# Kernel optimization log

Hardware: AMD Instinct MI355X
Metric: run time of the kernel (lower is better)

## Reference

```python
import jax, jax.numpy as jnp
import numpy as np

FD, FO, FK, H = 1024, 512, 128, 4
N = 32768


def setup_inputs() -> dict:
    key = jax.random.key(0)
    ks = jax.random.split(key, 8)
    s = 0.02
    return {
        "Xd": jax.random.normal(ks[0], (N, FD), dtype=jnp.float32),
        "Xo": jax.random.normal(ks[1], (N, FO), dtype=jnp.float32),
        "Wq": jax.random.normal(ks[2], (FO, FK * H), dtype=jnp.float32) * s,
        "bq": jnp.zeros((FK * H,), dtype=jnp.float32),
        "Wk": jax.random.normal(ks[3], (FD, FK * H), dtype=jnp.float32) * s,
        "bk": jnp.zeros((FK * H,), dtype=jnp.float32),
        "Wv": jax.random.normal(ks[4], (FD, FD * H), dtype=jnp.float32) * s,
        "bv": jnp.zeros((FD * H,), dtype=jnp.float32),
    }


def reference(Xd, Xo, Wq, bq, Wk, bk, Wv, bv):
    n = Xd.shape[0]
    Q = (Xo @ Wq + bq).reshape(n, H, FK)      # (n, H, fk)
    K = (Xd @ Wk + bk).reshape(n, H, FK)      # (n, H, fk)
    V = (Xd @ Wv + bv).reshape(n, H, FD)      # (n, H, fd)
    scores = jnp.sum(Q * K, axis=2, keepdims=True)  # (n, H, 1), no softmax
    Z = scores * V                              # (n, H, fd)
    Z = jnp.max(Z, axis=1)                      # max pooling over heads -> (n, fd)
    return Z  # dropout is identity in inference
```

## Files before the change

kernel.cpp:

```cpp
#include <hip/hip_runtime.h>

typedef __attribute__((ext_vector_type(8))) short short8;
typedef __attribute__((ext_vector_type(4))) float f32x4;

#define GLL16(gp, lp) __builtin_amdgcn_global_load_lds( \
    (__attribute__((address_space(1))) void*)(gp), \
    (__attribute__((address_space(3))) void*)(lp), 16, 0, 0)

__device__ __forceinline__ unsigned short f2b(float f) {
  unsigned int u = __builtin_bit_cast(unsigned int, f);
  u += 0x7fffu + ((u >> 16) & 1u);
  return (unsigned short)(u >> 16);
}
__device__ __forceinline__ float b2f(unsigned short s) {
  unsigned int u = ((unsigned int)s) << 16;
  return __builtin_bit_cast(float, u);
}

__global__ __launch_bounds__(256) void conv_k(const float* __restrict__ in,
                                              short8* __restrict__ out, long n8) {
  for (long i = (long)blockIdx.x * 256 + threadIdx.x; i < n8;
       i += (long)gridDim.x * 256) {
    const float4* p = (const float4*)in + 2 * i;
    float4 a = p[0], b = p[1];
    short8 v;
    v[0] = (short)f2b(a.x); v[1] = (short)f2b(a.y);
    v[2] = (short)f2b(a.z); v[3] = (short)f2b(a.w);
    v[4] = (short)f2b(b.x); v[5] = (short)f2b(b.y);
    v[6] = (short)f2b(b.z); v[7] = (short)f2b(b.w);
    out[i] = v;
  }
}

__global__ __launch_bounds__(256) void tconv_k(const float* __restrict__ in,
                                               unsigned short* __restrict__ out,
                                               int K, int C, int inter) {
  __shared__ float t[32][33];
  int k0 = blockIdx.x * 32, c0 = blockIdx.y * 32;
  int tx = threadIdx.x & 31, ty = threadIdx.x >> 5;
#pragma unroll
  for (int p = 0; p < 4; ++p)
    t[ty + p * 8][tx] = in[(size_t)(k0 + ty + p * 8) * C + c0 + tx];
  __syncthreads();
#pragma unroll
  for (int p = 0; p < 4; ++p) {
    int c = ty + p * 8;
    int gc = c0 + c;
    int orow = inter ? ((gc & 1023) * 4 + (gc >> 10)) : gc;
    out[(size_t)orow * K + k0 + tx] = f2b(t[tx][c]);
  }
}

template <int KD, int EPI>
__global__ __launch_bounds__(256) void gemm_k(
    const unsigned short* __restrict__ A, const unsigned short* __restrict__ Bt,
    const float* __restrict__ bias, const unsigned short* __restrict__ Qb,
    unsigned short* __restrict__ outb, float* __restrict__ sc,
    float* __restrict__ Z) {
  __shared__ __align__(16) unsigned short As[128 * 64];
  __shared__ __align__(16) unsigned short Bs[128 * 64];
  __shared__ float s_sc[512];
  __shared__ float sred[128][2];

  int tid = threadIdx.x;
  int bid = blockIdx.x;
  int ntile, mtile;
  if constexpr (EPI == 2) {
    int cpx = gridDim.x >> 3;
    int lb = (bid & 7) * cpx + (bid >> 3);
    ntile = lb & 31;
    mtile = lb >> 5;
  } else {
    ntile = bid & 3;
    mtile = bid >> 2;
  }
  int l = tid & 63, wid = tid >> 6, wm = wid >> 1, wn = wid & 1;
  int m0 = mtile * 128;

  if constexpr (EPI == 2) {
    for (int i = tid; i < 512; i += 256) s_sc[i] = sc[(size_t)m0 * 4 + i];
  }

  const unsigned short* Ab = A + (size_t)m0 * KD;
  const unsigned short* Bb = Bt + (size_t)ntile * 128 * KD;

  f32x4 zero = {0.f, 0.f, 0.f, 0.f};
  f32x4 acc[4][4];
#pragma unroll
  for (int m = 0; m < 4; ++m)
#pragma unroll
    for (int n = 0; n < 4; ++n) acc[m][n] = zero;

  for (int kt = 0; kt < KD / 64; ++kt) {
    const unsigned short* sA = Ab + kt * 64;
    const unsigned short* sB = Bb + kt * 64;
#pragma unroll
    for (int p = 0; p < 4; ++p) {
      int row = p * 32 + wid * 8 + (l >> 3);
      int sch = (l & 7) ^ (row & 7);
      GLL16((const char*)(sA + (size_t)row * KD) + sch * 16,
            (char*)As + p * 4096 + wid * 1024);
    }
#pragma unroll
    for (int p = 0; p < 4; ++p) {
      int row = p * 32 + wid * 8 + (l >> 3);
      int sch = (l & 7) ^ (row & 7);
      GLL16((const char*)(sB + (size_t)row * KD) + sch * 16,
            (char*)Bs + p * 4096 + wid * 1024);
    }
    __syncthreads();
#pragma unroll
    for (int ks = 0; ks < 2; ++ks) {
      short8 af[4], bfr[4];
#pragma unroll
      for (int m = 0; m < 4; ++m) {
        int row = wm * 64 + m * 16 + (l & 15);
        int kc = ks * 4 + (l >> 4);
        af[m] = *(const short8*)((const char*)As + row * 128 +
                                 ((kc ^ (row & 7)) << 4));
      }
#pragma unroll
      for (int n = 0; n < 4; ++n) {
        int row = wn * 64 + n * 16 + (l & 15);
        int kc = ks * 4 + (l >> 4);
        bfr[n] = *(const short8*)((const char*)Bs + row * 128 +
                                  ((kc ^ (row & 7)) << 4));
      }
#pragma unroll
      for (int m = 0; m < 4; ++m)
#pragma unroll
        for (int n = 0; n < 4; ++n)
          acc[m][n] = __builtin_amdgcn_mfma_f32_16x16x32_bf16(af[m], bfr[n],
                                                              acc[m][n], 0, 0, 0);
    }
    __syncthreads();
  }

  if constexpr (EPI == 0) {
#pragma unroll
    for (int n = 0; n < 4; ++n) {
      int col = ntile * 128 + wn * 64 + n * 16 + (l & 15);
      float bb = bias[col];
#pragma unroll
      for (int m = 0; m < 4; ++m) {
        int rowb = m0 + wm * 64 + m * 16 + ((l >> 4) << 2);
#pragma unroll
        for (int r = 0; r < 4; ++r)
          outb[(size_t)(rowb + r) * 512 + col] = f2b(acc[m][n][r] + bb);
      }
    }
  } else if constexpr (EPI == 1) {
    float part[4][4] = {};
#pragma unroll
    for (int n = 0; n < 4; ++n) {
      int col = ntile * 128 + wn * 64 + n * 16 + (l & 15);
      float bb = bias[col];
#pragma unroll
      for (int m = 0; m < 4; ++m) {
        int rowb = m0 + wm * 64 + m * 16 + ((l >> 4) << 2);
#pragma unroll
        for (int r = 0; r < 4; ++r) {
          float kv = acc[m][n][r] + bb;
          part[m][r] += kv * b2f(Qb[(size_t)(rowb + r) * 512 + col]);
        }
      }
    }
#pragma unroll
    for (int m = 0; m < 4; ++m)
#pragma unroll
      for (int r = 0; r < 4; ++r) {
        float s = part[m][r];
        s += __shfl_xor(s, 1);
        s += __shfl_xor(s, 2);
        s += __shfl_xor(s, 4);
        s += __shfl_xor(s, 8);
        if ((l & 15) == 0)
          sred[wm * 64 + m * 16 + ((l >> 4) << 2) + r][wn] = s;
      }
    __syncthreads();
    if (tid < 128) sc[(size_t)(m0 + tid) * 4 + ntile] = sred[tid][0] + sred[tid][1];
  } else {
    float* Zs = (float*)As;
#pragma unroll
    for (int n = 0; n < 4; ++n) {
      int pl = wn * 64 + n * 16 + (l & 15);
      int pg = ntile * 128 + pl;
      int h = pl & 3;
      float bb = bias[(pg & 3) * 1024 + (pg >> 2)];
#pragma unroll
      for (int m = 0; m < 4; ++m) {
        int rl = wm * 64 + m * 16 + ((l >> 4) << 2);
#pragma unroll
        for (int r = 0; r < 4; ++r) {
          float z = s_sc[(rl + r) * 4 + h] * (acc[m][n][r] + bb);
          z = fmaxf(z, __shfl_xor(z, 1));
          z = fmaxf(z, __shfl_xor(z, 2));
          if ((l & 3) == 0) Zs[(rl + r) * 32 + (pl >> 2)] = z;
        }
      }
    }
    __syncthreads();
#pragma unroll
    for (int p = 0; p < 4; ++p) {
      int idx = p * 1024 + tid * 4;
      int row = idx >> 5, d = idx & 31;
      f32x4 v = *(const f32x4*)&Zs[idx];
      *(f32x4*)&Z[(size_t)(m0 + row) * 1024 + ntile * 32 + d] = v;
    }
  }
}

__global__ __launch_bounds__(256) void naive_k(
    const float* __restrict__ Xd, const float* __restrict__ Xo,
    const float* __restrict__ Wq, const float* __restrict__ bq,
    const float* __restrict__ Wk, const float* __restrict__ bk,
    const float* __restrict__ Wv, const float* __restrict__ bv,
    float* __restrict__ Z) {
  int i = blockIdx.x, t = threadIdx.x;
  __shared__ float xd[1024], xo[512], s[4];
  for (int j = t; j < 1024; j += 256) xd[j] = Xd[(size_t)i * 1024 + j];
  for (int j = t; j < 512; j += 256) xo[j] = Xo[(size_t)i * 512 + j];
  if (t < 4) s[t] = 0.f;
  __syncthreads();
  for (int c = t; c < 512; c += 256) {
    float q = bq[c], k = bk[c];
    for (int j = 0; j < 512; ++j) q += xo[j] * Wq[(size_t)j * 512 + c];
    for (int j = 0; j < 1024; ++j) k += xd[j] * Wk[(size_t)j * 512 + c];
    atomicAdd(&s[c >> 7], q * k);
  }
  __syncthreads();
  for (int d = t; d < 1024; d += 256) {
    float z = -INFINITY;
    for (int h = 0; h < 4; ++h) {
      float v = bv[h * 1024 + d];
      for (int j = 0; j < 1024; ++j) v += xd[j] * Wv[(size_t)j * 4096 + h * 1024 + d];
      z = fmaxf(z, s[h] * v);
    }
    Z[(size_t)i * 1024 + d] = z;
  }
}

extern "C" void kernel_launch(void* const* d_in, const int* in_sizes, int n_in,
                              void* d_out, int out_size, void* d_ws, size_t ws_size,
                              hipStream_t stream) {
  const float* Xd = (const float*)d_in[0];
  const float* Xo = (const float*)d_in[1];
  const float* Wq = (const float*)d_in[2];
  const float* bq = (const float*)d_in[3];
  const float* Wk = (const float*)d_in[4];
  const float* bk = (const float*)d_in[5];
  const float* Wv = (const float*)d_in[6];
  const float* bv = (const float*)d_in[7];
  float* Z = (float*)d_out;
  long N = in_sizes[0] / 1024;

  size_t sz_Xd = (size_t)N * 1024 * 2, sz_Xo = (size_t)N * 512 * 2;
  size_t sz_Wq = (size_t)512 * 512 * 2, sz_Wk = (size_t)512 * 1024 * 2;
  size_t sz_Wv = (size_t)4096 * 1024 * 2;
  size_t sz_Qb = (size_t)N * 512 * 2, sz_sc = (size_t)N * 4 * 4;
  size_t o_Xo = sz_Xd, o_Wq = o_Xo + sz_Xo, o_Wk = o_Wq + sz_Wq,
         o_Wv = o_Wk + sz_Wk, o_Qb = o_Wv + sz_Wv, o_sc = o_Qb + sz_Qb;
  size_t need = o_sc + sz_sc;

  if (ws_size < need || (N % 128) != 0) {
    naive_k<<<(int)N, 256, 0, stream>>>(Xd, Xo, Wq, bq, Wk, bk, Wv, bv, Z);
    return;
  }

  char* w = (char*)d_ws;
  unsigned short* Xd_b = (unsigned short*)w;
  unsigned short* Xo_b = (unsigned short*)(w + o_Xo);
  unsigned short* Wq_t = (unsigned short*)(w + o_Wq);
  unsigned short* Wk_t = (unsigned short*)(w + o_Wk);
  unsigned short* Wv_p = (unsigned short*)(w + o_Wv);
  unsigned short* Qb   = (unsigned short*)(w + o_Qb);
  float* sc = (float*)(w + o_sc);

  conv_k<<<2048, 256, 0, stream>>>(Xd, (short8*)Xd_b, N * 1024 / 8);
  conv_k<<<2048, 256, 0, stream>>>(Xo, (short8*)Xo_b, N * 512 / 8);
  tconv_k<<<dim3(16, 16), 256, 0, stream>>>(Wq, Wq_t, 512, 512, 0);
  tconv_k<<<dim3(32, 16), 256, 0, stream>>>(Wk, Wk_t, 1024, 512, 0);
  tconv_k<<<dim3(32, 128), 256, 0, stream>>>(Wv, Wv_p, 1024, 4096, 1);

  int mt = (int)(N / 128);
  gemm_k<512, 0><<<mt * 4, 256, 0, stream>>>(Xo_b, Wq_t, bq, nullptr, Qb, nullptr, nullptr);
  gemm_k<1024, 1><<<mt * 4, 256, 0, stream>>>(Xd_b, Wk_t, bk, Qb, nullptr, sc, nullptr);
  gemm_k<1024, 2><<<mt * 32, 256, 0, stream>>>(Xd_b, Wv_p, bv, nullptr, nullptr, sc, Z);
}
```

Before: 565.7 us.

## Replace V GEMM with 256x256-tile double-buffered kernel using direct-to-LDS loads

The large V projection GEMM (N x 4096 x 1024) moves from a 128x128-tile, 256-thread kernel to a new 256x256-tile, 512-thread kernel. The new kernel double-buffers LDS tiles filled by global_load_lds, so the next K-step's loads overlap the current MFMAs, and raises MFMA wave priority with s_setprio. The larger tiles raise arithmetic intensity and cut redundant global reads of A and B. In exchange it uses more LDS (128KB of tiles) and more accumulator registers, limiting occupancy, and it now requires N to be a multiple of 256.

Measured after the change: 533.9 us. 5.6% less time.

```diff
diff --git a/kernel.cpp b/kernel.cpp
--- a/kernel.cpp
+++ b/kernel.cpp
@@ -51,35 +51,143 @@
   }
 }
 
+template <int KD>
+__global__ __launch_bounds__(512, 2) void gemm_v256_k(
+    const unsigned short* __restrict__ A, const unsigned short* __restrict__ Bt,
+    const float* __restrict__ bias, const float* __restrict__ sc,
+    float* __restrict__ Z) {
+  __shared__ __align__(16) unsigned short Ash[2][16384];
+  __shared__ __align__(16) unsigned short Bsh[2][16384];
+  __shared__ float s_sc[1024];
+
+  int tid = threadIdx.x;
+  int bid = blockIdx.x;
+  int cpx = gridDim.x >> 3;
+  int lb = (bid & 7) * cpx + (bid >> 3);
+  int mtile = lb >> 4, nt0 = lb & 15;
+  long m0 = (long)mtile * 256;
+  int l = tid & 63, wid = tid >> 6, wm = wid >> 2, wn = wid & 3;
+
+  for (int i = tid; i < 1024; i += 512) s_sc[i] = sc[m0 * 4 + i];
+
+  int rowg = tid >> 3;
+  int srcOff = rowg * (KD * 2) + (((tid & 7) ^ (rowg & 7)) << 4);
+  const char* aB = (const char*)(A + m0 * KD) + srcOff;
+  const char* bB = (const char*)(Bt + (long)nt0 * 256 * KD) + srcOff;
+  char* AshB = (char*)Ash;
+  char* BshB = (char*)Bsh;
+  int dstOff = wid * 1024;
+
+  auto stage = [&](int k, int bb) {
+#pragma unroll
+    for (int h = 0; h < 2; ++h)
+#pragma unroll
+      for (int s = 0; s < 2; ++s) {
+        int go = (h * 128 + s * 64) * (KD * 2) + k * 128;
+        int lo = bb * 32768 + h * 16384 + s * 8192 + dstOff;
+        GLL16(aB + go, AshB + lo);
+        GLL16(bB + go, BshB + lo);
+      }
+  };
+
+  f32x4 zero = {0.f, 0.f, 0.f, 0.f};
+  f32x4 acc[8][4];
+#pragma unroll
+  for (int m = 0; m < 8; ++m)
+#pragma unroll
+    for (int n = 0; n < 4; ++n) acc[m][n] = zero;
+
+  stage(0, 0);
+
+  const int NKT = KD / 64;
+  for (int kt = 0; kt < NKT; ++kt) {
+    int b = kt & 1;
+    asm volatile("s_waitcnt vmcnt(0)" ::: "memory");
+    __builtin_amdgcn_s_barrier();
+    __builtin_amdgcn_sched_barrier(0);
+    if (kt + 1 < NKT) stage(kt + 1, b ^ 1);
+
+    const char* Al = AshB + b * 32768;
+    const char* Bl = BshB + b * 32768;
+    int ar = l & 15;
+    int kc = l >> 4;
+    short8 bf[2][4], af[4];
+#pragma unroll
+    for (int ks = 0; ks < 2; ++ks) {
+#pragma unroll
+      for (int mh = 0; mh < 2; ++mh) {
+        if (mh == 0) {
+#pragma unroll
+          for (int n = 0; n < 4; ++n) {
+            int row = wn * 64 + n * 16 + ar;
+            int c = (ks * 4 + kc) ^ (row & 7);
+            bf[ks][n] = *(const short8*)(Bl + row * 128 + (c << 4));
+          }
+        }
+#pragma unroll
+        for (int m = 0; m < 4; ++m) {
+          int row = wm * 128 + mh * 64 + m * 16 + ar;
+          int c = (ks * 4 + kc) ^ (row & 7);
+          af[m] = *(const short8*)(Al + row * 128 + (c << 4));
+        }
+        __builtin_amdgcn_s_barrier();
+        __builtin_amdgcn_s_setprio(1);
+#pragma unroll
+        for (int m = 0; m < 4; ++m)
+#pragma unroll
+          for (int n = 0; n < 4; ++n)
+            acc[mh * 4 + m][n] = __builtin_amdgcn_mfma_f32_16x16x32_bf16(
+                af[m], bf[ks][n], acc[mh * 4 + m][n], 0, 0, 0);
+        __builtin_amdgcn_s_setprio(0);
+        __builtin_amdgcn_s_barrier();
+      }
+    }
+  }
+
+  __syncthreads();
+  float* Zs = (float*)AshB;
+#pragma unroll
+  for (int n = 0; n < 4; ++n) {
+    int pl = wn * 64 + n * 16 + (l & 15);
+    int pg = nt0 * 256 + pl;
+    int h = pl & 3;
+    float bb = bias[(pg & 3) * 1024 + (pg >> 2)];
+#pragma unroll
+    for (int mi = 0; mi < 8; ++mi) {
+      int rl = wm * 128 + mi * 16 + ((l >> 4) << 2);
+#pragma unroll
+      for (int r = 0; r < 4; ++r) {
+        float z = s_sc[(rl + r) * 4 + h] * (acc[mi][n][r] + bb);
+        z = fmaxf(z, __shfl_xor(z, 1));
+        z = fmaxf(z, __shfl_xor(z, 2));
+        if ((l & 3) == 0) Zs[(rl + r) * 64 + (pl >> 2)] = z;
+      }
+    }
+  }
+  __syncthreads();
+#pragma unroll
+  for (int it = 0; it < 8; ++it) {
+    int i = it * 512 + tid;
+    int row = i >> 4, d4 = i & 15;
+    f32x4 v = *(const f32x4*)&Zs[row * 64 + d4 * 4];
+    *(f32x4*)&Z[(m0 + row) * 1024 + nt0 * 64 + d4 * 4] = v;
+  }
+}
+
 template <int KD, int EPI>
 __global__ __launch_bounds__(256) void gemm_k(
     const unsigned short* __restrict__ A, const unsigned short* __restrict__ Bt,
     const float* __restrict__ bias, const unsigned short* __restrict__ Qb,
-    unsigned short* __restrict__ outb, float* __restrict__ sc,
-    float* __restrict__ Z) {
+    unsigned short* __restrict__ outb, float* __restrict__ sc) {
   __shared__ __align__(16) unsigned short As[128 * 64];
   __shared__ __align__(16) unsigned short Bs[128 * 64];
-  __shared__ float s_sc[512];
   __shared__ float sred[128][2];
 
   int tid = threadIdx.x;
   int bid = blockIdx.x;
-  int ntile, mtile;
-  if constexpr (EPI == 2) {
-    int cpx = gridDim.x >> 3;
-    int lb = (bid & 7) * cpx + (bid >> 3);
-    ntile = lb & 31;
-    mtile = lb >> 5;
-  } else {
-    ntile = bid & 3;
-    mtile = bid >> 2;
-  }
+  int ntile = bid & 3, mtile = bid >> 2;
   int l = tid & 63, wid = tid >> 6, wm = wid >> 1, wn = wid & 1;
   int m0 = mtile * 128;
-
-  if constexpr (EPI == 2) {
-    for (int i = tid; i < 512; i += 256) s_sc[i] = sc[(size_t)m0 * 4 + i];
-  }
 
   const unsigned short* Ab = A + (size_t)m0 * KD;
   const unsigned short* Bb = Bt + (size_t)ntile * 128 * KD;
@@ -149,7 +257,7 @@
           outb[(size_t)(rowb + r) * 512 + col] = f2b(acc[m][n][r] + bb);
       }
     }
-  } else if constexpr (EPI == 1) {
+  } else {
     float part[4][4] = {};
 #pragma unroll
     for (int n = 0; n < 4; ++n) {
@@ -179,34 +287,6 @@
       }
     __syncthreads();
     if (tid < 128) sc[(size_t)(m0 + tid) * 4 + ntile] = sred[tid][0] + sred[tid][1];
-  } else {
-    float* Zs = (float*)As;
-#pragma unroll
-    for (int n = 0; n < 4; ++n) {
-      int pl = wn * 64 + n * 16 + (l & 15);
-      int pg = ntile * 128 + pl;
-      int h = pl & 3;
-      float bb = bias[(pg & 3) * 1024 + (pg >> 2)];
-#pragma unroll
-      for (int m = 0; m < 4; ++m) {
-        int rl = wm * 64 + m * 16 + ((l >> 4) << 2);
-#pragma unroll
-        for (int r = 0; r < 4; ++r) {
-          float z = s_sc[(rl + r) * 4 + h] * (acc[m][n][r] + bb);
-          z = fmaxf(z, __shfl_xor(z, 1));
-          z = fmaxf(z, __shfl_xor(z, 2));
-          if ((l & 3) == 0) Zs[(rl + r) * 32 + (pl >> 2)] = z;
-        }
-      }
-    }
-    __syncthreads();
-#pragma unroll
-    for (int p = 0; p < 4; ++p) {
-      int idx = p * 1024 + tid * 4;
-      int row = idx >> 5, d = idx & 31;
-      f32x4 v = *(const f32x4*)&Zs[idx];
-      *(f32x4*)&Z[(size_t)(m0 + row) * 1024 + ntile * 32 + d] = v;
-    }
   }
 }
 
@@ -262,7 +342,7 @@
          o_Wv = o_Wk + sz_Wk, o_Qb = o_Wv + sz_Wv, o_sc = o_Qb + sz_Qb;
   size_t need = o_sc + sz_sc;
 
-  if (ws_size < need || (N % 128) != 0) {
+  if (ws_size < need || (N % 256) != 0) {
     naive_k<<<(int)N, 256, 0, stream>>>(Xd, Xo, Wq, bq, Wk, bk, Wv, bv, Z);
     return;
   }
@@ -283,7 +363,7 @@
   tconv_k<<<dim3(32, 128), 256, 0, stream>>>(Wv, Wv_p, 1024, 4096, 1);
 
   int mt = (int)(N / 128);
-  gemm_k<512, 0><<<mt * 4, 256, 0, stream>>>(Xo_b, Wq_t, bq, nullptr, Qb, nullptr, nullptr);
-  gemm_k<1024, 1><<<mt * 4, 256, 0, stream>>>(Xd_b, Wk_t, bk, Qb, nullptr, sc, nullptr);
-  gemm_k<1024, 2><<<mt * 32, 256, 0, stream>>>(Xd_b, Wv_p, bv, nullptr, nullptr, sc, Z);
-}
+  gemm_k<512, 0><<<mt * 4, 256, 0, stream>>>(Xo_b, Wq_t, bq, nullptr, Qb, nullptr);
+  gemm_k<1024, 1><<<mt * 4, 256, 0, stream>>>(Xd_b, Wk_t, bk, Qb, nullptr, sc);
+  gemm_v256_k<1024><<<(int)(N / 256) * 16, 512, 0, stream>>>(Xd_b, Wv_p, bv, sc, Z);
+}
```

## Pre-pack operands into MFMA fragment layout and load directly to registers

Applied to the files above, without the earlier changes.

Conversion kernels now write A and B in a fragment-major bf16 layout, so each lane's 16-byte MFMA operand sits contiguously in global memory. The GEMM drops shared-memory staging and barriers in the main loop, loading fragments straight into registers with software double-buffering. Tiles grow to 256x128 with 512 threads. Every operand is now fetched from global or L2 by each wave with no LDS reuse, which raises cache traffic and register pressure.

Result: slower. 707.8 us (+25.1%).

```diff
diff --git a/kernel.cpp b/kernel.cpp
--- a/kernel.cpp
+++ b/kernel.cpp
@@ -2,10 +2,6 @@
 
 typedef __attribute__((ext_vector_type(8))) short short8;
 typedef __attribute__((ext_vector_type(4))) float f32x4;
-
-#define GLL16(gp, lp) __builtin_amdgcn_global_load_lds( \
-    (__attribute__((address_space(1))) void*)(gp), \
-    (__attribute__((address_space(3))) void*)(lp), 16, 0, 0)
 
 __device__ __forceinline__ unsigned short f2b(float f) {
   unsigned int u = __builtin_bit_cast(unsigned int, f);
@@ -17,72 +13,96 @@
   return __builtin_bit_cast(float, u);
 }
 
-__global__ __launch_bounds__(256) void conv_k(const float* __restrict__ in,
-                                              short8* __restrict__ out, long n8) {
-  for (long i = (long)blockIdx.x * 256 + threadIdx.x; i < n8;
-       i += (long)gridDim.x * 256) {
-    const float4* p = (const float4*)in + 2 * i;
+__global__ __launch_bounds__(256) void pack_a_k(const float* __restrict__ in,
+                                                unsigned short* __restrict__ out, int K) {
+  int R = blockIdx.x, t = threadIdx.x;
+  int NS = K / 32;
+  for (int i = 0; i < K / 128; ++i) {
+    int c = t + 256 * i;
+    int S = c >> 6, l = c & 63;
+    int row = R * 16 + (l & 15);
+    int k = S * 32 + (l >> 4) * 8;
+    const float4* p = (const float4*)(in + (size_t)row * K + k);
     float4 a = p[0], b = p[1];
     short8 v;
     v[0] = (short)f2b(a.x); v[1] = (short)f2b(a.y);
     v[2] = (short)f2b(a.z); v[3] = (short)f2b(a.w);
     v[4] = (short)f2b(b.x); v[5] = (short)f2b(b.y);
     v[6] = (short)f2b(b.z); v[7] = (short)f2b(b.w);
-    out[i] = v;
-  }
-}
-
-__global__ __launch_bounds__(256) void tconv_k(const float* __restrict__ in,
-                                               unsigned short* __restrict__ out,
-                                               int K, int C, int inter) {
-  __shared__ float t[32][33];
-  int k0 = blockIdx.x * 32, c0 = blockIdx.y * 32;
-  int tx = threadIdx.x & 31, ty = threadIdx.x >> 5;
-#pragma unroll
-  for (int p = 0; p < 4; ++p)
-    t[ty + p * 8][tx] = in[(size_t)(k0 + ty + p * 8) * C + c0 + tx];
+    ((short8*)out)[(size_t)(R * NS + S) * 64 + l] = v;
+  }
+}
+
+template <int INTER>
+__global__ __launch_bounds__(256) void pack_b_k(const float* __restrict__ in,
+                                                unsigned short* __restrict__ out,
+                                                int K, int C) {
+  __shared__ float tl[128][17];
+  int P = blockIdx.x, kc = blockIdx.y, t = threadIdx.x;
+  int k0 = kc * 128;
+#pragma unroll
+  for (int ii = 0; ii < 2; ++ii) {
+    int id = t + 256 * ii;
+    int k = id >> 2, g = id & 3;
+    int cbase;
+    if (INTER) cbase = g * 1024 + P * 4;
+    else       cbase = P * 16 + g * 4;
+    float4 f = *(const float4*)(in + (size_t)(k0 + k) * C + cbase);
+#pragma unroll
+    for (int q = 0; q < 4; ++q) {
+      int pi = INTER ? (q * 4 + g) : (g * 4 + q);
+      tl[k][pi] = ((const float*)&f)[q];
+    }
+  }
   __syncthreads();
-#pragma unroll
-  for (int p = 0; p < 4; ++p) {
-    int c = ty + p * 8;
-    int gc = c0 + c;
-    int orow = inter ? ((gc & 1023) * 4 + (gc >> 10)) : gc;
-    out[(size_t)orow * K + k0 + tx] = f2b(t[tx][c]);
-  }
-}
-
-template <int KD, int EPI>
-__global__ __launch_bounds__(256) void gemm_k(
-    const unsigned short* __restrict__ A, const unsigned short* __restrict__ Bt,
+  int Sl = t >> 6, l = t & 63;
+  short8 v;
+#pragma unroll
+  for (int j = 0; j < 8; ++j)
+    v[j] = (short)f2b(tl[Sl * 32 + (l >> 4) * 8 + j][l & 15]);
+  int NS = K / 32;
+  ((short8*)out)[(size_t)(P * NS + kc * 4 + Sl) * 64 + l] = v;
+}
+
+template <int KD, int NTI, int EPI>
+__global__ __launch_bounds__(512, 3) void gemm_flat(
+    const unsigned short* __restrict__ Af, const unsigned short* __restrict__ Bf,
     const float* __restrict__ bias, const unsigned short* __restrict__ Qb,
     unsigned short* __restrict__ outb, float* __restrict__ sc,
     float* __restrict__ Z) {
-  __shared__ __align__(16) unsigned short As[128 * 64];
-  __shared__ __align__(16) unsigned short Bs[128 * 64];
-  __shared__ float s_sc[512];
-  __shared__ float sred[128][2];
+  constexpr int NS = KD / 32;
+  constexpr int SMB = (EPI == 2) ? (36864) : 2048;
+  __shared__ __align__(16) char smem[SMB];
 
   int tid = threadIdx.x;
   int bid = blockIdx.x;
-  int ntile, mtile;
+  int cpx = gridDim.x >> 3;
+  int lb = (bid & 7) * cpx + (bid >> 3);
+  int mtile = lb / NTI, nt = lb % NTI;
+  long m0 = (long)mtile * 256;
+  int l = tid & 63, wid = tid >> 6, wm = wid >> 1, wn = wid & 1;
+
+  float* s_sc = (float*)smem;
+  float* Zs = (float*)(smem + 4096);
+  float (*sred)[2] = (float(*)[2])smem;
+
   if constexpr (EPI == 2) {
-    int cpx = gridDim.x >> 3;
-    int lb = (bid & 7) * cpx + (bid >> 3);
-    ntile = lb & 31;
-    mtile = lb >> 5;
-  } else {
-    ntile = bid & 3;
-    mtile = bid >> 2;
-  }
-  int l = tid & 63, wid = tid >> 6, wm = wid >> 1, wn = wid & 1;
-  int m0 = mtile * 128;
-
-  if constexpr (EPI == 2) {
-    for (int i = tid; i < 512; i += 256) s_sc[i] = sc[(size_t)m0 * 4 + i];
-  }
-
-  const unsigned short* Ab = A + (size_t)m0 * KD;
-  const unsigned short* Bb = Bt + (size_t)ntile * 128 * KD;
+    for (int i = tid; i < 1024; i += 512) s_sc[i] = sc[m0 * 4 + i];
+  }
+
+  const char* Ab[4];
+  const char* Bb[4];
+#pragma unroll
+  for (int m = 0; m < 4; ++m) {
+    int R = (int)(m0 >> 4) + wm * 4 + m;
+    Ab[m] = (const char*)Af + (size_t)R * NS * 1024;
+  }
+#pragma unroll
+  for (int n = 0; n < 4; ++n) {
+    int P = nt * 8 + wn * 4 + n;
+    Bb[n] = (const char*)Bf + (size_t)P * NS * 1024;
+  }
+  int voff = l * 16;
 
   f32x4 zero = {0.f, 0.f, 0.f, 0.f};
   f32x4 acc[4][4];
@@ -91,77 +111,65 @@
 #pragma unroll
     for (int n = 0; n < 4; ++n) acc[m][n] = zero;
 
-  for (int kt = 0; kt < KD / 64; ++kt) {
-    const unsigned short* sA = Ab + kt * 64;
-    const unsigned short* sB = Bb + kt * 64;
-#pragma unroll
-    for (int p = 0; p < 4; ++p) {
-      int row = p * 32 + wid * 8 + (l >> 3);
-      int sch = (l & 7) ^ (row & 7);
-      GLL16((const char*)(sA + (size_t)row * KD) + sch * 16,
-            (char*)As + p * 4096 + wid * 1024);
-    }
-#pragma unroll
-    for (int p = 0; p < 4; ++p) {
-      int row = p * 32 + wid * 8 + (l >> 3);
-      int sch = (l & 7) ^ (row & 7);
-      GLL16((const char*)(sB + (size_t)row * KD) + sch * 16,
-            (char*)Bs + p * 4096 + wid * 1024);
-    }
-    __syncthreads();
-#pragma unroll
-    for (int ks = 0; ks < 2; ++ks) {
-      short8 af[4], bfr[4];
+#define LD4(dst, bases, add)                                              \
+  do {                                                                    \
+    _Pragma("unroll") for (int i_ = 0; i_ < 4; ++i_)                      \
+        dst[i_] = *(const short8*)(bases[i_] + voff + (add));             \
+  } while (0)
+#define MF(A_, B_)                                                        \
+  do {                                                                    \
+    _Pragma("unroll") for (int m_ = 0; m_ < 4; ++m_)                      \
+        _Pragma("unroll") for (int n_ = 0; n_ < 4; ++n_) acc[m_][n_] =    \
+            __builtin_amdgcn_mfma_f32_16x16x32_bf16(A_[m_], B_[n_],       \
+                                                    acc[m_][n_], 0, 0, 0);\
+  } while (0)
+
+  short8 a0[4], b0[4], a1[4], b1[4];
+  LD4(a0, Ab, 0);
+  LD4(b0, Bb, 0);
+  int off = 0;
+  for (int s = 0; s + 2 < NS; s += 2) {
+    LD4(a1, Ab, off + 1024);
+    LD4(b1, Bb, off + 1024);
+    MF(a0, b0);
+    LD4(a0, Ab, off + 2048);
+    LD4(b0, Bb, off + 2048);
+    MF(a1, b1);
+    off += 2048;
+  }
+  LD4(a1, Ab, off + 1024);
+  LD4(b1, Bb, off + 1024);
+  MF(a0, b0);
+  MF(a1, b1);
+#undef LD4
+#undef MF
+
+  if constexpr (EPI == 0) {
+#pragma unroll
+    for (int n = 0; n < 4; ++n) {
+      int col = nt * 128 + wn * 64 + n * 16 + (l & 15);
+      float bb = bias[col];
 #pragma unroll
       for (int m = 0; m < 4; ++m) {
-        int row = wm * 64 + m * 16 + (l & 15);
-        int kc = ks * 4 + (l >> 4);
-        af[m] = *(const short8*)((const char*)As + row * 128 +
-                                 ((kc ^ (row & 7)) << 4));
-      }
-#pragma unroll
-      for (int n = 0; n < 4; ++n) {
-        int row = wn * 64 + n * 16 + (l & 15);
-        int kc = ks * 4 + (l >> 4);
-        bfr[n] = *(const short8*)((const char*)Bs + row * 128 +
-                                  ((kc ^ (row & 7)) << 4));
-      }
-#pragma unroll
-      for (int m = 0; m < 4; ++m)
-#pragma unroll
-        for (int n = 0; n < 4; ++n)
-          acc[m][n] = __builtin_amdgcn_mfma_f32_16x16x32_bf16(af[m], bfr[n],
-                                                              acc[m][n], 0, 0, 0);
-    }
-    __syncthreads();
-  }
-
-  if constexpr (EPI == 0) {
-#pragma unroll
-    for (int n = 0; n < 4; ++n) {
-      int col = ntile * 128 + wn * 64 + n * 16 + (l & 15);
-      float bb = bias[col];
-#pragma unroll
-      for (int m = 0; m < 4; ++m) {
-        int rowb = m0 + wm * 64 + m * 16 + ((l >> 4) << 2);
+        long rowb = m0 + wm * 64 + m * 16 + ((l >> 4) << 2);
 #pragma unroll
         for (int r = 0; r < 4; ++r)
-          outb[(size_t)(rowb + r) * 512 + col] = f2b(acc[m][n][r] + bb);
+          outb[(rowb + r) * 512 + col] = f2b(acc[m][n][r] + bb);
       }
     }
   } else if constexpr (EPI == 1) {
     float part[4][4] = {};
 #pragma unroll
     for (int n = 0; n < 4; ++n) {
-      int col = ntile * 128 + wn * 64 + n * 16 + (l & 15);
+      int col = nt * 128 + wn * 64 + n * 16 + (l & 15);
       float bb = bias[col];
 #pragma unroll
       for (int m = 0; m < 4; ++m) {
-        int rowb = m0 + wm * 64 + m * 16 + ((l >> 4) << 2);
+        long rowb = m0 + wm * 64 + m * 16 + ((l >> 4) << 2);
 #pragma unroll
         for (int r = 0; r < 4; ++r) {
           float kv = acc[m][n][r] + bb;
-          part[m][r] += kv * b2f(Qb[(size_t)(rowb + r) * 512 + col]);
+          part[m][r] += kv * b2f(Qb[(rowb + r) * 512 + col]);
         }
       }
     }
@@ -178,14 +186,14 @@
           sred[wm * 64 + m * 16 + ((l >> 4) << 2) + r][wn] = s;
       }
     __syncthreads();
-    if (tid < 128) sc[(size_t)(m0 + tid) * 4 + ntile] = sred[tid][0] + sred[tid][1];
+    if (tid < 256) sc[(m0 + tid) * 4 + nt] = sred[tid][0] + sred[tid][1];
   } else {
-    float* Zs = (float*)As;
+    __syncthreads();
 #pragma unroll
     for (int n = 0; n < 4; ++n) {
       int pl = wn * 64 + n * 16 + (l & 15);
-      int pg = ntile * 128 + pl;
-      int h = pl & 3;
+      int pg = nt * 128 + pl;
+      int h = pg & 3;
       float bb = bias[(pg & 3) * 1024 + (pg >> 2)];
 #pragma unroll
       for (int m = 0; m < 4; ++m) {
@@ -201,11 +209,11 @@
     }
     __syncthreads();
 #pragma unroll
-    for (int p = 0; p < 4; ++p) {
-      int idx = p * 1024 + tid * 4;
-      int row = idx >> 5, d = idx & 31;
-      f32x4 v = *(const f32x4*)&Zs[idx];
-      *(f32x4*)&Z[(size_t)(m0 + row) * 1024 + ntile * 32 + d] = v;
+    for (int it = 0; it < 4; ++it) {
+      int i = it * 512 + tid;
+      int row = i >> 3, q = i & 7;
+      f32x4 v = *(const f32x4*)&Zs[row * 32 + q * 4];
+      *(f32x4*)&Z[(m0 + row) * 1024 + nt * 32 + q * 4] = v;
     }
   }
 }
@@ -262,28 +270,31 @@
          o_Wv = o_Wk + sz_Wk, o_Qb = o_Wv + sz_Wv, o_sc = o_Qb + sz_Qb;
   size_t need = o_sc + sz_sc;
 
-  if (ws_size < need || (N % 128) != 0) {
+  if (ws_size < need || (N % 256) != 0) {
     naive_k<<<(int)N, 256, 0, stream>>>(Xd, Xo, Wq, bq, Wk, bk, Wv, bv, Z);
     return;
   }
 
   char* w = (char*)d_ws;
-  unsigned short* Xd_b = (unsigned short*)w;
-  unsigned short* Xo_b = (unsigned short*)(w + o_Xo);
-  unsigned short* Wq_t = (unsigned short*)(w + o_Wq);
-  unsigned short* Wk_t = (unsigned short*)(w + o_Wk);
-  unsigned short* Wv_p = (unsigned short*)(w + o_Wv);
+  unsigned short* Xd_f = (unsigned short*)w;
+  unsigned short* Xo_f = (unsigned short*)(w + o_Xo);
+  unsigned short* Wq_f = (unsigned short*)(w + o_Wq);
+  unsigned short* Wk_f = (unsigned short*)(w + o_Wk);
+  unsigned short* Wv_f = (unsigned short*)(w + o_Wv);
   unsigned short* Qb   = (unsigned short*)(w + o_Qb);
   float* sc = (float*)(w + o_sc);
 
-  conv_k<<<2048, 256, 0, stream>>>(Xd, (short8*)Xd_b, N * 1024 / 8);
-  conv_k<<<2048, 256, 0, stream>>>(Xo, (short8*)Xo_b, N * 512 / 8);
-  tconv_k<<<dim3(16, 16), 256, 0, stream>>>(Wq, Wq_t, 512, 512, 0);
-  tconv_k<<<dim3(32, 16), 256, 0, stream>>>(Wk, Wk_t, 1024, 512, 0);
-  tconv_k<<<dim3(32, 128), 256, 0, stream>>>(Wv, Wv_p, 1024, 4096, 1);
-
-  int mt = (int)(N / 128);
-  gemm_k<512, 0><<<mt * 4, 256, 0, stream>>>(Xo_b, Wq_t, bq, nullptr, Qb, nullptr, nullptr);
-  gemm_k<1024, 1><<<mt * 4, 256, 0, stream>>>(Xd_b, Wk_t, bk, Qb, nullptr, sc, nullptr);
-  gemm_k<1024, 2><<<mt * 32, 256, 0, stream>>>(Xd_b, Wv_p, bv, nullptr, nullptr, sc, Z);
-}
+  pack_a_k<<<(int)(N / 16), 256, 0, stream>>>(Xd, Xd_f, 1024);
+  pack_a_k<<<(int)(N / 16), 256, 0, stream>>>(Xo, Xo_f, 512);
+  pack_b_k<0><<<dim3(32, 4), 256, 0, stream>>>(Wq, Wq_f, 512, 512);
+  pack_b_k<0><<<dim3(32, 8), 256, 0, stream>>>(Wk, Wk_f, 1024, 512);
+  pack_b_k<1><<<dim3(256, 8), 256, 0, stream>>>(Wv, Wv_f, 1024, 4096);
+
+  int mt = (int)(N / 256);
+  gemm_flat<512, 4, 0><<<mt * 4, 512, 0, stream>>>(Xo_f, Wq_f, bq, nullptr, Qb,
+                                                   nullptr, nullptr);
+  gemm_flat<1024, 4, 1><<<mt * 4, 512, 0, stream>>>(Xd_f, Wk_f, bk, Qb, nullptr,
+                                                    sc, nullptr);
+  gemm_flat<1024, 32, 2><<<mt * 32, 512, 0, stream>>>(Xd_f, Wv_f, bv, nullptr,
+                                                      nullptr, sc, Z);
+}
```

## Replace GEMM kernel with 256x256-tile, 8-wave, double-buffered pipelined MFMA kernel

Applied to the files above, without the earlier changes.

Replaces the 128x128 single-buffered GEMM with a 256x256-tile kernel that uses 512 threads and 128 KB of double-buffered LDS. Global-to-LDS loads for the next k-tile are interleaved with MFMA quadrants, using explicit vmcnt waits, raw barriers and s_setprio. The larger tile raises arithmetic intensity and the pipelining hides load latency. In exchange it needs more registers and LDS per block, which may limit occupancy. The fallback path now requires N divisible by 256.

After: 471.3 us. 1.2x faster.

```diff
diff --git a/kernel.cpp b/kernel.cpp
--- a/kernel.cpp
+++ b/kernel.cpp
@@ -51,161 +51,245 @@
   }
 }
 
-template <int KD, int EPI>
-__global__ __launch_bounds__(256) void gemm_k(
+template <int KD, int NTI, int EPI>
+__global__ __launch_bounds__(512, 2) void gemm_p(
     const unsigned short* __restrict__ A, const unsigned short* __restrict__ Bt,
     const float* __restrict__ bias, const unsigned short* __restrict__ Qb,
     unsigned short* __restrict__ outb, float* __restrict__ sc,
     float* __restrict__ Z) {
-  __shared__ __align__(16) unsigned short As[128 * 64];
-  __shared__ __align__(16) unsigned short Bs[128 * 64];
-  __shared__ float s_sc[512];
-  __shared__ float sred[128][2];
-
+  __shared__ __align__(16) char lds[131072];
+  __shared__ float s_sc[1024];
+
+  constexpr int NKT = KD / 64;
   int tid = threadIdx.x;
   int bid = blockIdx.x;
-  int ntile, mtile;
+  int cpx = gridDim.x >> 3;
+  int lb = (bid & 7) * cpx + (bid >> 3);
+  int mtile = lb / NTI, nt0 = lb % NTI;
+  long m0 = (long)mtile * 256;
+  int l = tid & 63, wid = tid >> 6, wm = wid >> 2, wn = wid & 3;
+
+  int rowg = tid >> 3;
+  int swz = (tid & 7) ^ (rowg & 7);
+  const char* aSrc = (const char*)(A + m0 * KD) + (long)rowg * (KD * 2) + swz * 16;
+  const char* bSrc = (const char*)(Bt + (long)nt0 * 256 * KD) + (long)rowg * (KD * 2) + swz * 16;
+  char* ldsb = (char*)lds;
+  int dstOff = wid * 1024;
+
+  auto stageA = [&](int hh, int tt) {
+    char* base = ldsb + ((tt & 1) * 32768 + hh * 16384) + dstOff;
+    const char* s = aSrc + (long)(hh * 128) * (KD * 2) + tt * 128;
+    GLL16(s, base);
+    GLL16(s + (long)64 * (KD * 2), base + 8192);
+  };
+  auto stageB = [&](int hh, int tt) {
+    char* base = ldsb + 65536 + ((tt & 1) * 32768 + hh * 16384) + dstOff;
+    const char* s = bSrc + (long)(hh * 128) * (KD * 2) + tt * 128;
+    GLL16(s, base);
+    GLL16(s + (long)64 * (KD * 2), base + 8192);
+  };
+
+  int ar = l & 15, kcl = l >> 4;
+  int x0 = ((kcl ^ (ar & 7)) << 4);
+  int x1 = (((4 | kcl) ^ (ar & 7)) << 4);
+  int thrA = (wm * 64 + ar) * 128;
+  int thrB = (wn * 32 + ar) * 128;
+
+  short8 aA[4][2], aB[4][2], b0[2][2], b1[2][2];
+
+#define RD_A(dst, slotoff)                                                  \
+  do {                                                                      \
+    const char* p_ = ldsb + (slotoff) + thrA;                               \
+    _Pragma("unroll") for (int m_ = 0; m_ < 4; ++m_) {                      \
+      dst[m_][0] = *(const short8*)(p_ + x0 + m_ * 2048);                   \
+      dst[m_][1] = *(const short8*)(p_ + x1 + m_ * 2048);                   \
+    }                                                                       \
+  } while (0)
+#define RD_B(dst, slotoff)                                                  \
+  do {                                                                      \
+    const char* p_ = ldsb + 65536 + (slotoff) + thrB;                       \
+    _Pragma("unroll") for (int n_ = 0; n_ < 2; ++n_) {                      \
+      dst[n_][0] = *(const short8*)(p_ + x0 + n_ * 2048);                   \
+      dst[n_][1] = *(const short8*)(p_ + x1 + n_ * 2048);                   \
+    }                                                                       \
+  } while (0)
+#define MFQ(q, am, bn)                                                      \
+  do {                                                                      \
+    __builtin_amdgcn_s_setprio(1);                                          \
+    _Pragma("unroll") for (int m_ = 0; m_ < 4; ++m_)                        \
+        _Pragma("unroll") for (int n_ = 0; n_ < 2; ++n_)                    \
+            _Pragma("unroll") for (int k_ = 0; k_ < 2; ++k_)                \
+                acc[q][m_ * 2 + n_] = __builtin_amdgcn_mfma_f32_16x16x32_bf16( \
+                    am[m_][k_], bn[n_][k_], acc[q][m_ * 2 + n_], 0, 0, 0);  \
+    __builtin_amdgcn_s_setprio(0);                                          \
+  } while (0)
+#define VM(n) asm volatile("s_waitcnt vmcnt(" #n ")" ::: "memory")
+#define BAR() __builtin_amdgcn_s_barrier()
+#define CLOB() asm volatile("" ::: "memory")
+
+  f32x4 zero = {0.f, 0.f, 0.f, 0.f};
+  f32x4 acc[4][8];
+#pragma unroll
+  for (int q = 0; q < 4; ++q)
+#pragma unroll
+    for (int f = 0; f < 8; ++f) acc[q][f] = zero;
+
+  stageA(0, 0); stageB(0, 0); stageB(1, 0); stageA(1, 0);
   if constexpr (EPI == 2) {
-    int cpx = gridDim.x >> 3;
-    int lb = (bid & 7) * cpx + (bid >> 3);
-    ntile = lb & 31;
-    mtile = lb >> 5;
-  } else {
-    ntile = bid & 3;
-    mtile = bid >> 2;
-  }
-  int l = tid & 63, wid = tid >> 6, wm = wid >> 1, wn = wid & 1;
-  int m0 = mtile * 128;
-
-  if constexpr (EPI == 2) {
-    for (int i = tid; i < 512; i += 256) s_sc[i] = sc[(size_t)m0 * 4 + i];
-  }
-
-  const unsigned short* Ab = A + (size_t)m0 * KD;
-  const unsigned short* Bb = Bt + (size_t)ntile * 128 * KD;
-
-  f32x4 zero = {0.f, 0.f, 0.f, 0.f};
-  f32x4 acc[4][4];
-#pragma unroll
-  for (int m = 0; m < 4; ++m)
-#pragma unroll
-    for (int n = 0; n < 4; ++n) acc[m][n] = zero;
-
-  for (int kt = 0; kt < KD / 64; ++kt) {
-    const unsigned short* sA = Ab + kt * 64;
-    const unsigned short* sB = Bb + kt * 64;
-#pragma unroll
-    for (int p = 0; p < 4; ++p) {
-      int row = p * 32 + wid * 8 + (l >> 3);
-      int sch = (l & 7) ^ (row & 7);
-      GLL16((const char*)(sA + (size_t)row * KD) + sch * 16,
-            (char*)As + p * 4096 + wid * 1024);
-    }
-#pragma unroll
-    for (int p = 0; p < 4; ++p) {
-      int row = p * 32 + wid * 8 + (l >> 3);
-      int sch = (l & 7) ^ (row & 7);
-      GLL16((const char*)(sB + (size_t)row * KD) + sch * 16,
-            (char*)Bs + p * 4096 + wid * 1024);
-    }
-    __syncthreads();
-#pragma unroll
-    for (int ks = 0; ks < 2; ++ks) {
-      short8 af[4], bfr[4];
-#pragma unroll
-      for (int m = 0; m < 4; ++m) {
-        int row = wm * 64 + m * 16 + (l & 15);
-        int kc = ks * 4 + (l >> 4);
-        af[m] = *(const short8*)((const char*)As + row * 128 +
-                                 ((kc ^ (row & 7)) << 4));
-      }
-#pragma unroll
-      for (int n = 0; n < 4; ++n) {
-        int row = wn * 64 + n * 16 + (l & 15);
-        int kc = ks * 4 + (l >> 4);
-        bfr[n] = *(const short8*)((const char*)Bs + row * 128 +
-                                  ((kc ^ (row & 7)) << 4));
-      }
-#pragma unroll
-      for (int m = 0; m < 4; ++m)
-#pragma unroll
-        for (int n = 0; n < 4; ++n)
-          acc[m][n] = __builtin_amdgcn_mfma_f32_16x16x32_bf16(af[m], bfr[n],
-                                                              acc[m][n], 0, 0, 0);
-    }
-    __syncthreads();
-  }
+    for (int i = tid; i < 1024; i += 512) s_sc[i] = sc[m0 * 4 + i];
+  }
+  VM(4); BAR(); CLOB();
+  RD_A(aA, 0);
+  RD_B(b0, 0);
+
+  for (int t = 0; t < NKT - 1; ++t) {
+    int aS = (t & 1) * 32768;
+    int bS = aS;
+    int aS2 = aS ^ 32768;
+    stageA(0, t + 1);
+    VM(4); BAR(); CLOB();
+    RD_B(b1, bS + 16384);
+    MFQ(0, aA, b0);
+    stageB(0, t + 1);
+    VM(4); BAR(); CLOB();
+    RD_A(aB, aS + 16384);
+    MFQ(1, aA, b1);
+    stageB(1, t + 1);
+    VM(4); BAR(); CLOB();
+    RD_A(aA, aS2);
+    MFQ(2, aB, b0);
+    stageA(1, t + 1);
+    VM(4); BAR(); CLOB();
+    RD_B(b0, aS2);
+    MFQ(3, aB, b1);
+  }
+  {
+    constexpr int t = NKT - 1;
+    int aS = (t & 1) * 32768;
+    VM(2); BAR(); CLOB();
+    RD_B(b1, aS + 16384);
+    MFQ(0, aA, b0);
+    VM(0); BAR(); CLOB();
+    RD_A(aB, aS + 16384);
+    MFQ(1, aA, b1);
+    MFQ(2, aB, b0);
+    MFQ(3, aB, b1);
+  }
+#undef RD_A
+#undef RD_B
+#undef MFQ
+#undef VM
+#undef BAR
+#undef CLOB
 
   if constexpr (EPI == 0) {
 #pragma unroll
-    for (int n = 0; n < 4; ++n) {
-      int col = ntile * 128 + wn * 64 + n * 16 + (l & 15);
-      float bb = bias[col];
-#pragma unroll
-      for (int m = 0; m < 4; ++m) {
-        int rowb = m0 + wm * 64 + m * 16 + ((l >> 4) << 2);
-#pragma unroll
-        for (int r = 0; r < 4; ++r)
-          outb[(size_t)(rowb + r) * 512 + col] = f2b(acc[m][n][r] + bb);
-      }
-    }
-  } else if constexpr (EPI == 1) {
-    float part[4][4] = {};
-#pragma unroll
-    for (int n = 0; n < 4; ++n) {
-      int col = ntile * 128 + wn * 64 + n * 16 + (l & 15);
-      float bb = bias[col];
-#pragma unroll
-      for (int m = 0; m < 4; ++m) {
-        int rowb = m0 + wm * 64 + m * 16 + ((l >> 4) << 2);
-#pragma unroll
-        for (int r = 0; r < 4; ++r) {
-          float kv = acc[m][n][r] + bb;
-          part[m][r] += kv * b2f(Qb[(size_t)(rowb + r) * 512 + col]);
+    for (int qm = 0; qm < 2; ++qm)
+#pragma unroll
+      for (int qn = 0; qn < 2; ++qn) {
+        int q = qm * 2 + qn;
+#pragma unroll
+        for (int n = 0; n < 2; ++n) {
+          int col = nt0 * 256 + qn * 128 + wn * 32 + n * 16 + (l & 15);
+          float bb = bias[col];
+#pragma unroll
+          for (int m = 0; m < 4; ++m) {
+            long rowb = m0 + qm * 128 + wm * 64 + m * 16 + ((l >> 4) << 2);
+#pragma unroll
+            for (int r = 0; r < 4; ++r)
+              outb[(rowb + r) * 512 + col] = f2b(acc[q][m * 2 + n][r] + bb);
+          }
         }
       }
-    }
-#pragma unroll
-    for (int m = 0; m < 4; ++m)
-#pragma unroll
-      for (int r = 0; r < 4; ++r) {
-        float s = part[m][r];
-        s += __shfl_xor(s, 1);
-        s += __shfl_xor(s, 2);
-        s += __shfl_xor(s, 4);
-        s += __shfl_xor(s, 8);
-        if ((l & 15) == 0)
-          sred[wm * 64 + m * 16 + ((l >> 4) << 2) + r][wn] = s;
+  } else if constexpr (EPI == 1) {
+    float part[2][2][4][4];
+#pragma unroll
+    for (int qm = 0; qm < 2; ++qm)
+#pragma unroll
+      for (int qn = 0; qn < 2; ++qn)
+#pragma unroll
+        for (int m = 0; m < 4; ++m)
+#pragma unroll
+          for (int r = 0; r < 4; ++r) part[qm][qn][m][r] = 0.f;
+#pragma unroll
+    for (int qm = 0; qm < 2; ++qm)
+#pragma unroll
+      for (int qn = 0; qn < 2; ++qn) {
+        int q = qm * 2 + qn;
+#pragma unroll
+        for (int n = 0; n < 2; ++n) {
+          int col = nt0 * 256 + qn * 128 + wn * 32 + n * 16 + (l & 15);
+          float bb = bias[col];
+#pragma unroll
+          for (int m = 0; m < 4; ++m) {
+            long rowb = m0 + qm * 128 + wm * 64 + m * 16 + ((l >> 4) << 2);
+#pragma unroll
+            for (int r = 0; r < 4; ++r) {
+              float kv = acc[q][m * 2 + n][r] + bb;
+              part[qm][qn][m][r] += kv * b2f(Qb[(rowb + r) * 512 + col]);
+            }
+          }
+        }
       }
     __syncthreads();
-    if (tid < 128) sc[(size_t)(m0 + tid) * 4 + ntile] = sred[tid][0] + sred[tid][1];
+    float (*sred)[2][4] = (float(*)[2][4])ldsb;
+#pragma unroll
+    for (int qm = 0; qm < 2; ++qm)
+#pragma unroll
+      for (int qn = 0; qn < 2; ++qn)
+#pragma unroll
+        for (int m = 0; m < 4; ++m)
+#pragma unroll
+          for (int r = 0; r < 4; ++r) {
+            float s = part[qm][qn][m][r];
+            s += __shfl_xor(s, 1);
+            s += __shfl_xor(s, 2);
+            s += __shfl_xor(s, 4);
+            s += __shfl_xor(s, 8);
+            if ((l & 15) == 0)
+              sred[qm * 128 + wm * 64 + m * 16 + ((l >> 4) << 2) + r][qn][wn] = s;
+          }
+    __syncthreads();
+    {
+      int row = tid >> 1, hh = tid & 1;
+      float v = sred[row][hh][0] + sred[row][hh][1] + sred[row][hh][2] +
+                sred[row][hh][3];
+      sc[(m0 + row) * 4 + nt0 * 2 + hh] = v;
+    }
   } else {
-    float* Zs = (float*)As;
-#pragma unroll
-    for (int n = 0; n < 4; ++n) {
-      int pl = wn * 64 + n * 16 + (l & 15);
-      int pg = ntile * 128 + pl;
-      int h = pl & 3;
-      float bb = bias[(pg & 3) * 1024 + (pg >> 2)];
-#pragma unroll
-      for (int m = 0; m < 4; ++m) {
-        int rl = wm * 64 + m * 16 + ((l >> 4) << 2);
-#pragma unroll
-        for (int r = 0; r < 4; ++r) {
-          float z = s_sc[(rl + r) * 4 + h] * (acc[m][n][r] + bb);
-          z = fmaxf(z, __shfl_xor(z, 1));
-          z = fmaxf(z, __shfl_xor(z, 2));
-          if ((l & 3) == 0) Zs[(rl + r) * 32 + (pl >> 2)] = z;
+    __syncthreads();
+    float* Zs = (float*)ldsb;
+#pragma unroll
+    for (int qm = 0; qm < 2; ++qm)
+#pragma unroll
+      for (int qn = 0; qn < 2; ++qn) {
+        int q = qm * 2 + qn;
+#pragma unroll
+        for (int n = 0; n < 2; ++n) {
+          int pl = qn * 128 + wn * 32 + n * 16 + (l & 15);
+          int pg = nt0 * 256 + pl;
+          int h = pl & 3;
+          float bb = bias[(pg & 3) * 1024 + (pg >> 2)];
+#pragma unroll
+          for (int m = 0; m < 4; ++m) {
+            int rl = qm * 128 + wm * 64 + m * 16 + ((l >> 4) << 2);
+#pragma unroll
+            for (int r = 0; r < 4; ++r) {
+              float z = s_sc[(rl + r) * 4 + h] * (acc[q][m * 2 + n][r] + bb);
+              z = fmaxf(z, __shfl_xor(z, 1));
+              z = fmaxf(z, __shfl_xor(z, 2));
+              if ((l & 3) == 0) Zs[(rl + r) * 64 + (pl >> 2)] = z;
+            }
+          }
         }
       }
-    }
     __syncthreads();
 #pragma unroll
-    for (int p = 0; p < 4; ++p) {
-      int idx = p * 1024 + tid * 4;
-      int row = idx >> 5, d = idx & 31;
-      f32x4 v = *(const f32x4*)&Zs[idx];
-      *(f32x4*)&Z[(size_t)(m0 + row) * 1024 + ntile * 32 + d] = v;
+    for (int it = 0; it < 8; ++it) {
+      int i = it * 512 + tid;
+      int row = i >> 4, d4 = i & 15;
+      f32x4 v = *(const f32x4*)&Zs[row * 64 + d4 * 4];
+      *(f32x4*)&Z[(m0 + row) * 1024 + nt0 * 64 + d4 * 4] = v;
     }
   }
 }
@@ -262,7 +346,7 @@
          o_Wv = o_Wk + sz_Wk, o_Qb = o_Wv + sz_Wv, o_sc = o_Qb + sz_Qb;
   size_t need = o_sc + sz_sc;
 
-  if (ws_size < need || (N % 128) != 0) {
+  if (ws_size < need || (N % 256) != 0) {
     naive_k<<<(int)N, 256, 0, stream>>>(Xd, Xo, Wq, bq, Wk, bk, Wv, bv, Z);
     return;
   }
@@ -282,8 +366,11 @@
   tconv_k<<<dim3(32, 16), 256, 0, stream>>>(Wk, Wk_t, 1024, 512, 0);
   tconv_k<<<dim3(32, 128), 256, 0, stream>>>(Wv, Wv_p, 1024, 4096, 1);
 
-  int mt = (int)(N / 128);
-  gemm_k<512, 0><<<mt * 4, 256, 0, stream>>>(Xo_b, Wq_t, bq, nullptr, Qb, nullptr, nullptr);
-  gemm_k<1024, 1><<<mt * 4, 256, 0, stream>>>(Xd_b, Wk_t, bk, Qb, nullptr, sc, nullptr);
-  gemm_k<1024, 2><<<mt * 32, 256, 0, stream>>>(Xd_b, Wv_p, bv, nullptr, nullptr, sc, Z);
-}
+  int mt = (int)(N / 256);
+  gemm_p<512, 2, 0><<<mt * 2, 512, 0, stream>>>(Xo_b, Wq_t, bq, nullptr, Qb,
+                                                nullptr, nullptr);
+  gemm_p<1024, 2, 1><<<mt * 2, 512, 0, stream>>>(Xd_b, Wk_t, bk, Qb, nullptr,
+                                                 sc, nullptr);
+  gemm_p<1024, 16, 2><<<mt * 16, 512, 0, stream>>>(Xd_b, Wv_p, bv, nullptr,
+                                                   nullptr, sc, Z);
+}
```
